# Kernel tuning notes

Hardware: AMD Instinct MI355X
Metric: run time of the kernel (lower is better)

## Reference

```python
import jax, jax.numpy as jnp
import numpy as np

B, T, DIM = 4, 2048, 512
H = 8
HD = DIM // H  # 64
ALPHA = 100.0
EPS = 1e-10


def setup_inputs() -> dict:
    key = jax.random.key(0)
    k1, k2, k3, k4 = jax.random.split(key, 4)
    x = jax.random.normal(k1, (B, T, DIM), dtype=jnp.float32)
    # torch Linear weights; stored here as [in, out] for x @ W
    W_qkv = jax.random.normal(k2, (DIM, 2 * DIM), dtype=jnp.float32) * (DIM ** -0.5)
    W_proj = jax.random.normal(k3, (DIM, DIM), dtype=jnp.float32) * (DIM ** -0.5)
    b_proj = jax.random.normal(k4, (DIM,), dtype=jnp.float32) * 0.01
    return {"x": x, "W_qkv": W_qkv, "W_proj": W_proj, "b_proj": b_proj}


def reference(x, W_qkv, W_proj, b_proj):
    b, t, dim = x.shape
    qkv = x @ W_qkv                                   # [b,t,2*dim]
    # einops 'b t (d k h) -> k b h t d' with k=2, h=H: innermost grouping order (d, k, h)
    qkv = qkv.reshape(b, t, HD, 2, H)                 # [b,t,d,2,h]
    qk = jnp.transpose(qkv[:, :, :, 0, :], (0, 3, 1, 2))  # [b,h,t,d]
    v = jnp.transpose(qkv[:, :, :, 1, :], (0, 3, 1, 2))   # [b,h,t,d]
    q = qk  # q == k
    qsq = jnp.sum(q * q, axis=-1)                     # [b,h,t]
    dots = jnp.einsum('bhtd,bhsd->bhts', q, q)        # [b,h,t,s]
    score = -(qsq[..., :, None] + qsq[..., None, :] - 2.0 * dots)
    # Frobenius norm of q over (t,d) per (b,h)
    a = jnp.sqrt(jnp.sum(q * q, axis=(2, 3), keepdims=True))  # [b,h,1,1]
    x_norm = jnp.sqrt(jnp.sum(x * x, axis=-1))                 # [b,t]
    bmax = jnp.max(x_norm, axis=1).reshape(b, 1, 1, 1)         # [b,1,1,1]
    scale = 1.0 / (a * bmax + EPS)
    attn = jax.nn.softmax(ALPHA * score * scale, axis=-1)      # [b,h,t,s]
    out = jnp.einsum('bhts,bhsd->bhtd', attn, v)               # [b,h,t,d]
    out = jnp.transpose(out, (0, 2, 1, 3)).reshape(b, t, dim)  # b t (h d)
    return out @ W_proj + b_proj
```

## Files before the change

### kernel.cpp

```cpp
#include <hip/hip_runtime.h>
#include <hip/hip_bf16.h>

#define BB 4
#define TT 2048
#define DIM 512
#define NH 8
#define HD 64
#define NROW (BB*TT)
#define BH (BB*NH)

typedef unsigned short u16;
typedef unsigned int u32;
typedef __attribute__((ext_vector_type(8))) short bf16x8;
typedef __attribute__((ext_vector_type(8))) unsigned short u16x8;
typedef __attribute__((ext_vector_type(4))) float f32x4;
typedef __attribute__((ext_vector_type(16))) float f32x16;
typedef __attribute__((ext_vector_type(4))) unsigned short u16x4;
typedef __attribute__((ext_vector_type(2))) unsigned int u32x2;

static __device__ __forceinline__ float bf2f(u16 u) {
    return __uint_as_float(((u32)u) << 16);
}
static __device__ __forceinline__ u16 f2bf(float f) {
    u32 u = __float_as_uint(f);
    u32 r = (u + 0x7FFFu + ((u >> 16) & 1u)) >> 16;
    return (u16)r;
}
static __device__ __forceinline__ u32 cvtpk(float a, float b) {
    union { __hip_bfloat162 h2; u32 u; } cv;
    cv.h2 = __float22bfloat162_rn(make_float2(a, b));
    return cv.u;
}
static __device__ __forceinline__ void gll16(const u16* g, u16* l) {
    __builtin_amdgcn_global_load_lds(
        (const __attribute__((address_space(1))) unsigned int*)g,
        (__attribute__((address_space(3))) unsigned int*)l,
        16, 0, 0);
}

__global__ __launch_bounds__(256) void prep_kernel(
    const float* __restrict__ x, u16* __restrict__ x16, u32* __restrict__ bmaxsq,
    const float* __restrict__ Wqkv, u16* __restrict__ Wtq,
    const float* __restrict__ Wproj, u16* __restrict__ Wtp)
{
    const int bid = blockIdx.x;
    const int tid = threadIdx.x;
    __shared__ u16 t[32][33];
    __shared__ float red[4];

    if (bid < 256) {
        const int row = bid * 32 + (tid >> 3);
        const int b = (bid * 32) >> 11;
        const float* xr = x   + (size_t)row * DIM + (tid & 7) * 64;
        u16*        xo  = x16 + (size_t)row * DIM + (tid & 7) * 64;
        float s = 0.0f;
        #pragma unroll
        for (int j = 0; j < 8; ++j) {
            float4 a = *(const float4*)(xr + j*8);
            float4 c = *(const float4*)(xr + j*8 + 4);
            s += a.x*a.x + a.y*a.y + a.z*a.z + a.w*a.w;
            s += c.x*c.x + c.y*c.y + c.z*c.z + c.w*c.w;
            u16x8 pk;
            pk[0]=f2bf(a.x); pk[1]=f2bf(a.y); pk[2]=f2bf(a.z); pk[3]=f2bf(a.w);
            pk[4]=f2bf(c.x); pk[5]=f2bf(c.y); pk[6]=f2bf(c.z); pk[7]=f2bf(c.w);
            *(u16x8*)(xo + j*8) = pk;
        }
        #pragma unroll
        for (int off = 1; off < 8; off <<= 1) s += __shfl_xor(s, off, 64);
        float m = s;
        #pragma unroll
        for (int off = 8; off < 64; off <<= 1) m = fmaxf(m, __shfl_xor(m, off, 64));
        if ((tid & 63) == 0) red[tid >> 6] = m;
        __syncthreads();
        if (tid == 0) {
            float mx = fmaxf(fmaxf(red[0], red[1]), fmaxf(red[2], red[3]));
            atomicMax(&bmaxsq[b], __float_as_uint(mx));
        }
    } else {
        const float* in; u16* outp; int K, N, tb;
        if (bid < 768) { in = Wqkv; outp = Wtq; K = 512; N = 1024; tb = bid - 256; }
        else           { in = Wproj; outp = Wtp; K = 512; N = 512;  tb = bid - 768; }
        const int ntiles = N >> 5;
        const int bx = tb % ntiles, by = tb / ntiles;
        const int n0 = bx * 32, k0 = by * 32;
        const int tx = tid & 31, ty = tid >> 5;
        #pragma unroll
        for (int i = 0; i < 32; i += 8)
            t[ty + i][tx] = f2bf(in[(size_t)(k0 + ty + i) * N + n0 + tx]);
        __syncthreads();
        #pragma unroll
        for (int i = 0; i < 32; i += 8)
            outp[(size_t)(n0 + ty + i) * K + k0 + tx] = t[tx][ty + i];
    }
}

#define LDG 72
__global__ __launch_bounds__(256) void qkv_mfma(
    const u16* __restrict__ x16, const u16* __restrict__ Wt,
    u16* __restrict__ q16, u16* __restrict__ vt16)
{
    const int tid = threadIdx.x, lane = tid & 63, w = tid >> 6;
    const int li = lane & 15, quad = lane >> 4;
    const int mb = blockIdx.x >> 3, nb = blockIdx.x & 7;
    const int row0 = mb * 128, n0 = nb * 128;
    const int b = row0 >> 11;
    const int wm = w >> 1, wn = w & 1;

    __shared__ __align__(16) u16 as[128 * LDG];
    __shared__ __align__(16) u16 bs[128 * LDG];

    f32x4 acc[4][4];
    #pragma unroll
    for (int mi = 0; mi < 4; ++mi)
        #pragma unroll
        for (int ni = 0; ni < 4; ++ni) acc[mi][ni] = f32x4{0.f,0.f,0.f,0.f};

    for (int k0 = 0; k0 < DIM; k0 += 64) {
        __syncthreads();
        #pragma unroll
        for (int it = 0; it < 4; ++it) {
            int id = it * 256 + tid;
            int r = id >> 3, c = id & 7;
            *(bf16x8*)&as[r*LDG + c*8] =
                *(const bf16x8*)(x16 + (size_t)(row0 + r)*DIM + k0 + c*8);
            *(bf16x8*)&bs[r*LDG + c*8] =
                *(const bf16x8*)(Wt  + (size_t)(n0  + r)*DIM + k0 + c*8);
        }
        __syncthreads();

        bf16x8 af[4][2], bfr[4][2];
        #pragma unroll
        for (int mi = 0; mi < 4; ++mi) {
            const u16* p = &as[(wm*64 + mi*16 + li)*LDG + quad*8];
            af[mi][0] = *(const bf16x8*)p;
            af[mi][1] = *(const bf16x8*)(p + 32);
        }
        #pragma unroll
        for (int ni = 0; ni < 4; ++ni) {
            const u16* p = &bs[(wn*64 + ni*16 + li)*LDG + quad*8];
            bfr[ni][0] = *(const bf16x8*)p;
            bfr[ni][1] = *(const bf16x8*)(p + 32);
        }
        #pragma unroll
        for (int mi = 0; mi < 4; ++mi)
            #pragma unroll
            for (int ni = 0; ni < 4; ++ni) {
                acc[mi][ni] = __builtin_amdgcn_mfma_f32_16x16x32_bf16(
                    af[mi][0], bfr[ni][0], acc[mi][ni], 0, 0, 0);
                acc[mi][ni] = __builtin_amdgcn_mfma_f32_16x16x32_bf16(
                    af[mi][1], bfr[ni][1], acc[mi][ni], 0, 0, 0);
            }
    }

    const int h = li & 7;
    const bool isv = ((li >> 3) & 1) != 0;
    #pragma unroll
    for (int ni = 0; ni < 4; ++ni) {
        int col0 = n0 + wn*64 + ni*16;
        int d = col0 >> 4;
        #pragma unroll
        for (int mi = 0; mi < 4; ++mi) {
            int t0 = (row0 & (TT-1)) + wm*64 + mi*16 + quad*4;
            if (!isv) {
                u16* dst = q16 + ((size_t)(b*NH + h)*TT + t0)*HD + d;
                #pragma unroll
                for (int r = 0; r < 4; ++r)
                    dst[(size_t)r * HD] = f2bf(acc[mi][ni][r]);
            } else {
                u16x4 pk;
                pk.x = f2bf(acc[mi][ni][0]); pk.y = f2bf(acc[mi][ni][1]);
                pk.z = f2bf(acc[mi][ni][2]); pk.w = f2bf(acc[mi][ni][3]);
                *(u16x4*)(vt16 + ((size_t)(b*NH + h)*HD + d)*TT + t0) = pk;
            }
        }
    }
}

__global__ __launch_bounds__(256) void proj_mfma(
    const u16* __restrict__ ao16, const u16* __restrict__ Wt,
    const float* __restrict__ bp, float* __restrict__ out)
{
    const int tid = threadIdx.x, lane = tid & 63, w = tid >> 6;
    const int li = lane & 15, quad = lane >> 4;
    const int mb = blockIdx.x >> 2, nb = blockIdx.x & 3;
    const int row0 = mb * 128, n0 = nb * 128;
    const int wm = w >> 1, wn = w & 1;

    __shared__ __align__(16) u16 as[128 * LDG];
    __shared__ __align__(16) u16 bs[128 * LDG];

    f32x4 acc[4][4];
    #pragma unroll
    for (int mi = 0; mi < 4; ++mi)
        #pragma unroll
        for (int ni = 0; ni < 4; ++ni) acc[mi][ni] = f32x4{0.f,0.f,0.f,0.f};

    for (int k0 = 0; k0 < DIM; k0 += 64) {
        __syncthreads();
        #pragma unroll
        for (int it = 0; it < 4; ++it) {
            int id = it * 256 + tid;
            int r = id >> 3, c = id & 7;
            *(bf16x8*)&as[r*LDG + c*8] =
                *(const bf16x8*)(ao16 + (size_t)(row0 + r)*DIM + k0 + c*8);
            *(bf16x8*)&bs[r*LDG + c*8] =
                *(const bf16x8*)(Wt   + (size_t)(n0  + r)*DIM + k0 + c*8);
        }
        __syncthreads();

        bf16x8 af[4][2], bfr[4][2];
        #pragma unroll
        for (int mi = 0; mi < 4; ++mi) {
            const u16* p = &as[(wm*64 + mi*16 + li)*LDG + quad*8];
            af[mi][0] = *(const bf16x8*)p;
            af[mi][1] = *(const bf16x8*)(p + 32);
        }
        #pragma unroll
        for (int ni = 0; ni < 4; ++ni) {
            const u16* p = &bs[(wn*64 + ni*16 + li)*LDG + quad*8];
            bfr[ni][0] = *(const bf16x8*)p;
            bfr[ni][1] = *(const bf16x8*)(p + 32);
        }
        #pragma unroll
        for (int mi = 0; mi < 4; ++mi)
            #pragma unroll
            for (int ni = 0; ni < 4; ++ni) {
                acc[mi][ni] = __builtin_amdgcn_mfma_f32_16x16x32_bf16(
                    af[mi][0], bfr[ni][0], acc[mi][ni], 0, 0, 0);
                acc[mi][ni] = __builtin_amdgcn_mfma_f32_16x16x32_bf16(
                    af[mi][1], bfr[ni][1], acc[mi][ni], 0, 0, 0);
            }
    }

    #pragma unroll
    for (int ni = 0; ni < 4; ++ni) {
        int col = n0 + wn*64 + ni*16 + li;
        float bias = bp[col];
        #pragma unroll
        for (int mi = 0; mi < 4; ++mi) {
            int r0 = row0 + wm*64 + mi*16 + quad*4;
            #pragma unroll
            for (int r = 0; r < 4; ++r)
                out[(size_t)(r0 + r)*DIM + col] = acc[mi][ni][r] + bias;
        }
    }
}

__global__ __launch_bounds__(256) void qsq_kernel(
    const u16* __restrict__ q16, float* __restrict__ qsq, float* __restrict__ asq)
{
    const int tid = threadIdx.x;
    const int bh = blockIdx.x >> 3;
    const int r0 = (blockIdx.x & 7) * 256;
    const u16* qb = q16 + ((size_t)bh * TT + r0) * HD;

    float tot = 0.0f;
    #pragma unroll
    for (int i = 0; i < 8; ++i) {
        int row = i * 32 + (tid >> 3);
        u16x8 v = *(const u16x8*)(qb + (size_t)row * HD + (tid & 7) * 8);
        float s = 0.0f;
        #pragma unroll
        for (int j = 0; j < 8; ++j) { float f = bf2f(v[j]); s += f * f; }
        tot += s;
        #pragma unroll
        for (int off = 1; off < 8; off <<= 1) s += __shfl_xor(s, off, 64);
        if ((tid & 7) == 0) qsq[(size_t)bh * TT + r0 + row] = s;
    }
    __shared__ float red[4];
    #pragma unroll
    for (int off = 32; off > 0; off >>= 1) tot += __shfl_down(tot, off, 64);
    if ((tid & 63) == 0) red[tid >> 6] = tot;
    __syncthreads();
    if (tid == 0) atomicAdd(&asq[bh], red[0] + red[1] + red[2] + red[3]);
}

__global__ __launch_bounds__(256, 2) void attn_kernel(
    const u16* __restrict__ q16, const u16* __restrict__ vt16,
    const float* __restrict__ qsq, const float* __restrict__ asq,
    const u32* __restrict__ bmaxsq, u16* __restrict__ ao16)
{
    const int tid = threadIdx.x;
    const int lane = tid & 63, w = tid >> 6;
    const int l31 = lane & 31, hf = lane >> 5;
    const int l7 = lane & 7;
    const int ws = w & 1;
    const int p  = w >> 1;
    const int bh = blockIdx.x >> 4;
    const int qtile = blockIdx.x & 15;
    const int b = bh >> 3, head = bh & 7;

    __shared__ __align__(16) u16 smem[36864];
    u16* ksA = smem;
    u16* vtA = smem + 16384;
    float* cq = (float*)(smem + 32768);

    const u16* qgp = q16  + (size_t)bh * TT * HD;
    const u16* vgp = vt16 + (size_t)bh * HD * TT;
    const float* qsqg = qsq + (size_t)bh * TT;

    float cf;
    {
        float a  = sqrtf(asq[bh]);
        float bm = sqrtf(__uint_as_float(bmaxsq[b]));
        cf = (100.0f * 1.44269504089f) / (a * bm + 1e-10f);
    }
    const float c2 = 2.0f * cf;

    const int qt0 = qtile * 128 + p * 64;
    bf16x8 qf[2][4];
    #pragma unroll
    for (int qg = 0; qg < 2; ++qg) {
        const u16* qrow = qgp + (size_t)(qt0 + qg*32 + l31) * HD + hf * 8;
        #pragma unroll
        for (int kc = 0; kc < 4; ++kc)
            qf[qg][kc] = *(const bf16x8*)(qrow + kc * 16);
    }

    const int ci = tid * 8;
    f32x4 cqa = *(const f32x4*)(qsqg + ci);
    f32x4 cqb = *(const f32x4*)(qsqg + ci + 4);

    int slot[4];
    #pragma unroll
    for (int kc = 0; kc < 4; ++kc) slot[kc] = (((2*kc + hf) ^ l7) << 3);

    const int rk = tid >> 3;
    const int ck = (tid & 7) ^ (rk & 7);
    const u16* kstg = qgp + (size_t)rk * HD + ck * 8;
    const u16* vstg = vgp + (size_t)rk * TT + ck * 8;
    const int lb0 = w * 512;
    const int lb1 = 2048 + w * 512;

    auto stagePair = [&](int sb, int t0g) {
        #pragma unroll
        for (int ts = 0; ts < 2; ++ts) {
            const u16* kp = kstg + (size_t)(t0g + ts) * 64 * HD;
            const u16* vp = vstg + (t0g + ts) * 64;
            u16* kb = ksA + (sb + ts) * 4096;
            u16* vb = vtA + (sb + ts) * 4096;
            gll16(kp,                 kb + lb0);
            gll16(kp + 32 * HD,       kb + lb1);
            gll16(vp,                 vb + lb0);
            gll16(vp + (size_t)32*TT, vb + lb1);
        }
    };

    bf16x8 onesf;
    {
        union { u16 a[8]; bf16x8 v; } o;
        #pragma unroll
        for (int i = 0; i < 8; ++i) o.a[i] = 0x3F80;
        onesf = o.v;
    }

    f32x16 oacc[2][2], osum[2];
    #pragma unroll
    for (int qg = 0; qg < 2; ++qg) {
        #pragma unroll
        for (int r = 0; r < 16; ++r) { oacc[qg][0][r] = 0.f; oacc[qg][1][r] = 0.f; osum[qg][r] = 0.f; }
    }

    auto tile_compute = [&](const u16* __restrict__ ksb,
                            const u16* __restrict__ vtb, int s0) {
        bf16x8 pa[2][4];
        #pragma unroll
        for (int sc = 0; sc < 2; ++sc) {
            const u16* kbase = ksb + sc * 2048 + l31 * 64;
            bf16x8 kf0 = *(const bf16x8*)(kbase + slot[0]);
            bf16x8 kf1 = *(const bf16x8*)(kbase + slot[1]);
            bf16x8 kf2 = *(const bf16x8*)(kbase + slot[2]);
            bf16x8 kf3 = *(const bf16x8*)(kbase + slot[3]);
            f32x4 cq4[4];
            #pragma unroll
            for (int g = 0; g < 4; ++g)
                cq4[g] = *(const f32x4*)&cq[s0 + sc*32 + g*8 + hf*4];
            #pragma unroll
            for (int qg = 0; qg < 2; ++qg) {
                f32x16 acc;
                #pragma unroll
                for (int r = 0; r < 16; ++r) acc[r] = 0.0f;
                __builtin_amdgcn_s_setprio(1);
                acc = __builtin_amdgcn_mfma_f32_32x32x16_bf16(kf0, qf[qg][0], acc, 0, 0, 0);
                acc = __builtin_amdgcn_mfma_f32_32x32x16_bf16(kf1, qf[qg][1], acc, 0, 0, 0);
                acc = __builtin_amdgcn_mfma_f32_32x32x16_bf16(kf2, qf[qg][2], acc, 0, 0, 0);
                acc = __builtin_amdgcn_mfma_f32_32x32x16_bf16(kf3, qf[qg][3], acc, 0, 0, 0);
                __builtin_amdgcn_s_setprio(0);
                float pv[16];
                #pragma unroll
                for (int g = 0; g < 4; ++g) {
                    pv[4*g+0] = __builtin_amdgcn_exp2f(fmaf(c2, acc[4*g+0], -cq4[g][0]));
                    pv[4*g+1] = __builtin_amdgcn_exp2f(fmaf(c2, acc[4*g+1], -cq4[g][1]));
                    pv[4*g+2] = __builtin_amdgcn_exp2f(fmaf(c2, acc[4*g+2], -cq4[g][2]));
                    pv[4*g+3] = __builtin_amdgcn_exp2f(fmaf(c2, acc[4*g+3], -cq4[g][3]));
                }
                #pragma unroll
                for (int kh = 0; kh < 2; ++kh) {
                    u32 A0 = cvtpk(pv[8*kh+0], pv[8*kh+1]);
                    u32 B0 = cvtpk(pv[8*kh+4], pv[8*kh+5]);
                    u32 A1 = cvtpk(pv[8*kh+2], pv[8*kh+3]);
                    u32 B1 = cvtpk(pv[8*kh+6], pv[8*kh+7]);
                    u32x2 r0 = __builtin_amdgcn_permlane32_swap(A0, B0, false, false);
                    u32x2 r1 = __builtin_amdgcn_permlane32_swap(A1, B1, false, false);
                    union { u32 u[4]; bf16x8 v; } pw;
                    pw.u[0] = r0.x; pw.u[1] = r1.x; pw.u[2] = r0.y; pw.u[3] = r1.y;
                    pa[qg][sc*2 + kh] = pw.v;
                }
            }
        }
        #pragma unroll
        for (int kc = 0; kc < 4; ++kc) {
            bf16x8 vf0 = *(const bf16x8*)(vtb + (0*32 + l31) * 64 + slot[kc]);
            bf16x8 vf1 = *(const bf16x8*)(vtb + (1*32 + l31) * 64 + slot[kc]);
            __builtin_amdgcn_s_setprio(1);
            #pragma unroll
            for (int qg = 0; qg < 2; ++qg) {
                oacc[qg][0] = __builtin_amdgcn_mfma_f32_32x32x16_bf16(
                    pa[qg][kc], vf0, oacc[qg][0], 0, 0, 0);
                oacc[qg][1] = __builtin_amdgcn_mfma_f32_32x32x16_bf16(
                    pa[qg][kc], vf1, oacc[qg][1], 0, 0, 0);
                osum[qg] = __builtin_amdgcn_mfma_f32_32x32x16_bf16(
                    pa[qg][kc], onesf, osum[qg], 0, 0, 0);
            }
            __builtin_amdgcn_s_setprio(0);
        }
    };

    stagePair(0, 0);
    stagePair(2, 2);
    *(f32x4*)&cq[ci]     = cqa * cf;
    *(f32x4*)&cq[ci + 4] = cqb * cf;
    asm volatile("s_waitcnt lgkmcnt(0)" ::: "memory");
    __builtin_amdgcn_s_barrier();

    #pragma unroll 2
    for (int m = 0; m < 15; ++m) {
        asm volatile("s_waitcnt vmcnt(8)" ::: "memory");
        __builtin_amdgcn_s_barrier();
        const int sb = (m & 1) * 2;
        tile_compute(ksA + (sb + ws) * 4096, vtA + (sb + ws) * 4096,
                     (2*m + ws) * 64);
        __builtin_amdgcn_s_barrier();
        if (m <= 13) stagePair(sb, 2*(m + 2));
    }
    asm volatile("s_waitcnt vmcnt(0)" ::: "memory");
    __builtin_amdgcn_s_barrier();
    tile_compute(ksA + (2 + ws) * 4096, vtA + (2 + ws) * 4096,
                 (30 + ws) * 64);
    __builtin_amdgcn_s_barrier();

    float* cmb = (float*)smem;
    float* myc = cmb + p * 6144 + lane * 96;
    if (ws == 1) {
        #pragma unroll
        for (int qg = 0; qg < 2; ++qg) {
            #pragma unroll
            for (int dh = 0; dh < 2; ++dh)
                #pragma unroll
                for (int v4 = 0; v4 < 4; ++v4)
                    *(f32x4*)(myc + (qg*2 + dh)*16 + v4*4) =
                        f32x4{oacc[qg][dh][v4*4+0], oacc[qg][dh][v4*4+1],
                              oacc[qg][dh][v4*4+2], oacc[qg][dh][v4*4+3]};
            #pragma unroll
            for (int v4 = 0; v4 < 4; ++v4)
                *(f32x4*)(myc + 64 + qg*16 + v4*4) =
                    f32x4{osum[qg][v4*4+0], osum[qg][v4*4+1],
                          osum[qg][v4*4+2], osum[qg][v4*4+3]};
        }
    }
    asm volatile("s_waitcnt lgkmcnt(0)" ::: "memory");
    __builtin_amdgcn_s_barrier();
    if (ws == 0) {
        #pragma unroll
        for (int qg = 0; qg < 2; ++qg) {
            #pragma unroll
            for (int dh = 0; dh < 2; ++dh)
                #pragma unroll
                for (int r = 0; r < 16; ++r)
                    oacc[qg][dh][r] += myc[(qg*2 + dh)*16 + r];
            #pragma unroll
            for (int r = 0; r < 16; ++r)
                osum[qg][r] += myc[64 + qg*16 + r];
        }
        #pragma unroll
        for (int qg = 0; qg < 2; ++qg) {
            float inv[16];
            #pragma unroll
            for (int r = 0; r < 16; ++r) inv[r] = 1.0f / osum[qg][r];
            #pragma unroll
            for (int dh = 0; dh < 2; ++dh)
                #pragma unroll
                for (int g = 0; g < 4; ++g)
                    #pragma unroll
                    for (int r0 = 0; r0 < 4; ++r0) {
                        int t = qt0 + qg*32 + g*8 + hf*4 + r0;
                        ao16[((size_t)(b*TT + t))*DIM + head*HD + dh*32 + l31] =
                            f2bf(oacc[qg][dh][g*4 + r0] * inv[g*4 + r0]);
                    }
        }
    }
}

extern "C" void kernel_launch(void* const* d_in, const int* in_sizes, int n_in,
                              void* d_out, int out_size, void* d_ws, size_t ws_size,
                              hipStream_t stream)
{
    const float* x     = (const float*)d_in[0];
    const float* Wqkv  = (const float*)d_in[1];
    const float* Wproj = (const float*)d_in[2];
    const float* bproj = (const float*)d_in[3];
    float* out = (float*)d_out;

    char* ws = (char*)d_ws;
    const size_t MB = 1024*1024;
    u16*   q16  = (u16*)(ws);
    u16*   vt16 = (u16*)(ws + 8*MB);
    u16*   ao16 = (u16*)(ws + 16*MB);
    u16*   x16  = (u16*)(ws + 24*MB);
    u16*   Wtq  = (u16*)(ws + 32*MB);
    u16*   Wtp  = (u16*)(ws + 33*MB);
    float* qsq  = (float*)(ws + 34*MB);
    float* asq  = (float*)(ws + 34*MB + 262144);
    u32* bmaxsq = (u32*)(ws + 34*MB + 262144 + 128);

    (void)in_sizes; (void)n_in; (void)out_size; (void)ws_size;

    hipMemsetAsync(ws + 34*MB + 262144, 0, 144, stream);

    prep_kernel<<<1024, 256, 0, stream>>>(x, x16, bmaxsq, Wqkv, Wtq, Wproj, Wtp);

    qkv_mfma<<<64*8, 256, 0, stream>>>(x16, Wtq, q16, vt16);

    qsq_kernel<<<BH*8, 256, 0, stream>>>(q16, qsq, asq);

    attn_kernel<<<BH*16, 256, 0, stream>>>(q16, vt16, qsq, asq, bmaxsq, ao16);

    proj_mfma<<<64*4, 256, 0, stream>>>(ao16, Wtp, bproj, out);
}
```

Before: 132.8 us.

## Fold key-norm bias into MFMA accumulator init and use direct-to-LDS swizzled GEMM loads

The attention kernel stops keeping a per-key qsq table in shared memory and applying an fmaf before each exp2. Instead it builds a split-bf16 (hi+lo) bias row and runs one extra MFMA against a ones vector, then uses the result as the initial accumulator of the QK^T product, so the exp argument becomes a single multiply. The QKV and projection GEMMs replace padded LDS staging through registers with global-to-LDS direct loads (gll16) into an XOR-swizzled unpadded layout. This aims to cut VALU work and LDS usage in attention and register traffic in the GEMMs. The cost is an extra MFMA per 32-key chunk and a full vmcnt(0) wait before each GEMM k-step.

```diff
diff --git a/kernel.cpp b/kernel.cpp
--- a/kernel.cpp
+++ b/kernel.cpp
@@ -94,7 +94,6 @@
     }
 }
 
-#define LDG 72
 __global__ __launch_bounds__(256) void qkv_mfma(
     const u16* __restrict__ x16, const u16* __restrict__ Wt,
     u16* __restrict__ q16, u16* __restrict__ vt16)
@@ -106,8 +105,17 @@
     const int b = row0 >> 11;
     const int wm = w >> 1, wn = w & 1;
 
-    __shared__ __align__(16) u16 as[128 * LDG];
-    __shared__ __align__(16) u16 bs[128 * LDG];
+    __shared__ __align__(16) u16 as[128 * 64];
+    __shared__ __align__(16) u16 bs[128 * 64];
+
+    const int rstg = tid >> 3;
+    const int cstg = ((tid & 7) ^ (rstg & 7)) * 8;
+    const u16* xa = x16 + (size_t)(row0 + rstg) * DIM + cstg;
+    const u16* wb = Wt  + (size_t)(n0  + rstg) * DIM + cstg;
+    const int ldb = w * 512;
+
+    const int fs0 = ((quad)     ^ (li & 7)) << 3;
+    const int fs1 = ((quad + 4) ^ (li & 7)) << 3;
 
     f32x4 acc[4][4];
     #pragma unroll
@@ -119,27 +127,24 @@
         __syncthreads();
         #pragma unroll
         for (int it = 0; it < 4; ++it) {
-            int id = it * 256 + tid;
-            int r = id >> 3, c = id & 7;
-            *(bf16x8*)&as[r*LDG + c*8] =
-                *(const bf16x8*)(x16 + (size_t)(row0 + r)*DIM + k0 + c*8);
-            *(bf16x8*)&bs[r*LDG + c*8] =
-                *(const bf16x8*)(Wt  + (size_t)(n0  + r)*DIM + k0 + c*8);
-        }
+            gll16(xa + k0 + (size_t)it * 32 * DIM, as + it * 2048 + ldb);
+            gll16(wb + k0 + (size_t)it * 32 * DIM, bs + it * 2048 + ldb);
+        }
+        asm volatile("s_waitcnt vmcnt(0)" ::: "memory");
         __syncthreads();
 
         bf16x8 af[4][2], bfr[4][2];
         #pragma unroll
         for (int mi = 0; mi < 4; ++mi) {
-            const u16* p = &as[(wm*64 + mi*16 + li)*LDG + quad*8];
-            af[mi][0] = *(const bf16x8*)p;
-            af[mi][1] = *(const bf16x8*)(p + 32);
+            const u16* p = &as[(wm*64 + mi*16 + li) * 64];
+            af[mi][0] = *(const bf16x8*)(p + fs0);
+            af[mi][1] = *(const bf16x8*)(p + fs1);
         }
         #pragma unroll
         for (int ni = 0; ni < 4; ++ni) {
-            const u16* p = &bs[(wn*64 + ni*16 + li)*LDG + quad*8];
-            bfr[ni][0] = *(const bf16x8*)p;
-            bfr[ni][1] = *(const bf16x8*)(p + 32);
+            const u16* p = &bs[(wn*64 + ni*16 + li) * 64];
+            bfr[ni][0] = *(const bf16x8*)(p + fs0);
+            bfr[ni][1] = *(const bf16x8*)(p + fs1);
         }
         #pragma unroll
         for (int mi = 0; mi < 4; ++mi)
@@ -186,8 +191,17 @@
     const int row0 = mb * 128, n0 = nb * 128;
     const int wm = w >> 1, wn = w & 1;
 
-    __shared__ __align__(16) u16 as[128 * LDG];
-    __shared__ __align__(16) u16 bs[128 * LDG];
+    __shared__ __align__(16) u16 as[128 * 64];
+    __shared__ __align__(16) u16 bs[128 * 64];
+
+    const int rstg = tid >> 3;
+    const int cstg = ((tid & 7) ^ (rstg & 7)) * 8;
+    const u16* xa = ao16 + (size_t)(row0 + rstg) * DIM + cstg;
+    const u16* wb = Wt   + (size_t)(n0  + rstg) * DIM + cstg;
+    const int ldb = w * 512;
+
+    const int fs0 = ((quad)     ^ (li & 7)) << 3;
+    const int fs1 = ((quad + 4) ^ (li & 7)) << 3;
 
     f32x4 acc[4][4];
     #pragma unroll
@@ -199,27 +213,24 @@
         __syncthreads();
         #pragma unroll
         for (int it = 0; it < 4; ++it) {
-            int id = it * 256 + tid;
-            int r = id >> 3, c = id & 7;
-            *(bf16x8*)&as[r*LDG + c*8] =
-                *(const bf16x8*)(ao16 + (size_t)(row0 + r)*DIM + k0 + c*8);
-            *(bf16x8*)&bs[r*LDG + c*8] =
-                *(const bf16x8*)(Wt   + (size_t)(n0  + r)*DIM + k0 + c*8);
-        }
+            gll16(xa + k0 + (size_t)it * 32 * DIM, as + it * 2048 + ldb);
+            gll16(wb + k0 + (size_t)it * 32 * DIM, bs + it * 2048 + ldb);
+        }
+        asm volatile("s_waitcnt vmcnt(0)" ::: "memory");
         __syncthreads();
 
         bf16x8 af[4][2], bfr[4][2];
         #pragma unroll
         for (int mi = 0; mi < 4; ++mi) {
-            const u16* p = &as[(wm*64 + mi*16 + li)*LDG + quad*8];
-            af[mi][0] = *(const bf16x8*)p;
-            af[mi][1] = *(const bf16x8*)(p + 32);
+            const u16* p = &as[(wm*64 + mi*16 + li) * 64];
+            af[mi][0] = *(const bf16x8*)(p + fs0);
+            af[mi][1] = *(const bf16x8*)(p + fs1);
         }
         #pragma unroll
         for (int ni = 0; ni < 4; ++ni) {
-            const u16* p = &bs[(wn*64 + ni*16 + li)*LDG + quad*8];
-            bfr[ni][0] = *(const bf16x8*)p;
-            bfr[ni][1] = *(const bf16x8*)(p + 32);
+            const u16* p = &bs[(wn*64 + ni*16 + li) * 64];
+            bfr[ni][0] = *(const bf16x8*)(p + fs0);
+            bfr[ni][1] = *(const bf16x8*)(p + fs1);
         }
         #pragma unroll
         for (int mi = 0; mi < 4; ++mi)
@@ -290,10 +301,9 @@
     const int qtile = blockIdx.x & 15;
     const int b = bh >> 3, head = bh & 7;
 
-    __shared__ __align__(16) u16 smem[36864];
+    __shared__ __align__(16) u16 smem[32768];
     u16* ksA = smem;
     u16* vtA = smem + 16384;
-    float* cq = (float*)(smem + 32768);
 
     const u16* qgp = q16  + (size_t)bh * TT * HD;
     const u16* vgp = vt16 + (size_t)bh * HD * TT;
@@ -316,10 +326,6 @@
         for (int kc = 0; kc < 4; ++kc)
             qf[qg][kc] = *(const bf16x8*)(qrow + kc * 16);
     }
-
-    const int ci = tid * 8;
-    f32x4 cqa = *(const f32x4*)(qsqg + ci);
-    f32x4 cqb = *(const f32x4*)(qsqg + ci + 4);
 
     int slot[4];
     #pragma unroll
@@ -363,23 +369,32 @@
 
     auto tile_compute = [&](const u16* __restrict__ ksb,
                             const u16* __restrict__ vtb, int s0) {
+        float qs0 = qsqg[s0 + l31];
+        float qs1 = qsqg[s0 + 32 + l31];
         bf16x8 pa[2][4];
         #pragma unroll
         for (int sc = 0; sc < 2; ++sc) {
+            float vneg = -0.5f * (sc ? qs1 : qs0);
+            u16 bh16 = f2bf(vneg);
+            u16 bl16 = f2bf(vneg - bf2f(bh16));
+            union { u16 a[8]; bf16x8 v; } cqa_;
+            #pragma unroll
+            for (int i = 0; i < 8; ++i) cqa_.a[i] = 0;
+            cqa_.a[0] = hf ? (u16)0 : bh16;
+            cqa_.a[1] = hf ? (u16)0 : bl16;
+            f32x16 cqacc;
+            #pragma unroll
+            for (int r = 0; r < 16; ++r) cqacc[r] = 0.0f;
+            cqacc = __builtin_amdgcn_mfma_f32_32x32x16_bf16(cqa_.v, onesf, cqacc, 0, 0, 0);
+
             const u16* kbase = ksb + sc * 2048 + l31 * 64;
             bf16x8 kf0 = *(const bf16x8*)(kbase + slot[0]);
             bf16x8 kf1 = *(const bf16x8*)(kbase + slot[1]);
             bf16x8 kf2 = *(const bf16x8*)(kbase + slot[2]);
             bf16x8 kf3 = *(const bf16x8*)(kbase + slot[3]);
-            f32x4 cq4[4];
-            #pragma unroll
-            for (int g = 0; g < 4; ++g)
-                cq4[g] = *(const f32x4*)&cq[s0 + sc*32 + g*8 + hf*4];
             #pragma unroll
             for (int qg = 0; qg < 2; ++qg) {
-                f32x16 acc;
-                #pragma unroll
-                for (int r = 0; r < 16; ++r) acc[r] = 0.0f;
+                f32x16 acc = cqacc;
                 __builtin_amdgcn_s_setprio(1);
                 acc = __builtin_amdgcn_mfma_f32_32x32x16_bf16(kf0, qf[qg][0], acc, 0, 0, 0);
                 acc = __builtin_amdgcn_mfma_f32_32x32x16_bf16(kf1, qf[qg][1], acc, 0, 0, 0);
@@ -389,10 +404,10 @@
                 float pv[16];
                 #pragma unroll
                 for (int g = 0; g < 4; ++g) {
-                    pv[4*g+0] = __builtin_amdgcn_exp2f(fmaf(c2, acc[4*g+0], -cq4[g][0]));
-                    pv[4*g+1] = __builtin_amdgcn_exp2f(fmaf(c2, acc[4*g+1], -cq4[g][1]));
-                    pv[4*g+2] = __builtin_amdgcn_exp2f(fmaf(c2, acc[4*g+2], -cq4[g][2]));
-                    pv[4*g+3] = __builtin_amdgcn_exp2f(fmaf(c2, acc[4*g+3], -cq4[g][3]));
+                    pv[4*g+0] = __builtin_amdgcn_exp2f(c2 * acc[4*g+0]);
+                    pv[4*g+1] = __builtin_amdgcn_exp2f(c2 * acc[4*g+1]);
+                    pv[4*g+2] = __builtin_amdgcn_exp2f(c2 * acc[4*g+2]);
+                    pv[4*g+3] = __builtin_amdgcn_exp2f(c2 * acc[4*g+3]);
                 }
                 #pragma unroll
                 for (int kh = 0; kh < 2; ++kh) {
@@ -428,10 +443,6 @@
 
     stagePair(0, 0);
     stagePair(2, 2);
-    *(f32x4*)&cq[ci]     = cqa * cf;
-    *(f32x4*)&cq[ci + 4] = cqb * cf;
-    asm volatile("s_waitcnt lgkmcnt(0)" ::: "memory");
-    __builtin_amdgcn_s_barrier();
 
     #pragma unroll 2
     for (int m = 0; m < 15; ++m) {
```

Result: slower. 136.8 us (+3.0%).
